# Performance work log

Hardware: AMD Instinct MI355X
Metric: run time of the kernel (lower is better)

Reference implementation:

```python
import jax, jax.numpy as jnp
import numpy as np
from jax import lax

H = 64  # hidden_size

def _lstm_layer(x, w_ih, w_hh, b_ih, b_hh):
    # x: (B, T, in). PyTorch gate order [i, f, g, o]; gates = x@W_ih^T + h@W_hh^T + b_ih + b_hh.
    B, T, _ = x.shape
    xw = jnp.einsum('bti,gi->btg', x, w_ih) + (b_ih + b_hh)  # (B, T, 4H), input projection hoisted out of scan

    def step(carry, xw_t):
        h, c = carry
        gates = xw_t + h @ w_hh.T                     # (B, 4H)
        i, f, g, o = jnp.split(gates, 4, axis=-1)
        i = jax.nn.sigmoid(i)
        f = jax.nn.sigmoid(f)
        g = jnp.tanh(g)
        o = jax.nn.sigmoid(o)
        c = f * c + i * g
        h = o * jnp.tanh(c)
        return (h, c), h

    h0 = jnp.zeros((B, H), dtype=x.dtype)
    c0 = jnp.zeros((B, H), dtype=x.dtype)
    (h_n, _), hs = lax.scan(step, (h0, c0), jnp.swapaxes(xw, 0, 1))  # hs: (T, B, H)
    return jnp.swapaxes(hs, 0, 1), h_n


def setup_inputs() -> dict:
    key = jax.random.key(0)
    ks = jax.random.split(key, 12)
    s = 1.0 / np.sqrt(H)  # PyTorch LSTM init scale
    return {
        'x':     jax.random.normal(ks[0], (2048, 512, 4), dtype=jnp.float32),
        'w_ih0': jax.random.uniform(ks[1], (4 * H, 4), jnp.float32, -s, s),
        'w_hh0': jax.random.uniform(ks[2], (4 * H, H), jnp.float32, -s, s),
        'b_ih0': jax.random.uniform(ks[3], (4 * H,), jnp.float32, -s, s),
        'b_hh0': jax.random.uniform(ks[4], (4 * H,), jnp.float32, -s, s),
        'w_ih1': jax.random.uniform(ks[5], (4 * H, H), jnp.float32, -s, s),
        'w_hh1': jax.random.uniform(ks[6], (4 * H, H), jnp.float32, -s, s),
        'b_ih1': jax.random.uniform(ks[7], (4 * H,), jnp.float32, -s, s),
        'b_hh1': jax.random.uniform(ks[8], (4 * H,), jnp.float32, -s, s),
        'fc_w':  jax.random.uniform(ks[9], (H, H), jnp.float32, -s, s),
        'fc_b':  jax.random.uniform(ks[10], (H,), jnp.float32, -s, s),
    }


def reference(x, w_ih0, w_hh0, b_ih0, b_hh0, w_ih1, w_hh1, b_ih1, b_hh1, fc_w, fc_b):
    # 2-layer LSTM (eval mode: inter-layer dropout inactive), take last layer's final hidden,
    # then Linear + tanh.
    h1_seq, _ = _lstm_layer(x, w_ih0, w_hh0, b_ih0, b_hh0)
    _, h_n = _lstm_layer(h1_seq, w_ih1, w_hh1, b_ih1, b_hh1)
    return jnp.tanh(h_n @ fc_w.T + fc_b)
```

## Files before the change

kernel.cpp:

```cpp
#include <hip/hip_runtime.h>


#define HID 64
#define TSTEPS 512
#define MB 8
#define BLK 512
#define HSTR 72
#define LOG2E  1.4426950408889634f
#define LOG2E2 2.8853900817779268f

typedef _Float16 f16;
typedef _Float16 half8 __attribute__((ext_vector_type(8)));
typedef _Float16 half4 __attribute__((ext_vector_type(4)));
typedef float f32x4 __attribute__((ext_vector_type(4)));

__device__ __forceinline__ float sig2(float y) {
    return __builtin_amdgcn_rcpf(1.0f + __builtin_amdgcn_exp2f(-y));
}
__device__ __forceinline__ float tanh2(float y) {
    return fmaf(2.0f, __builtin_amdgcn_rcpf(1.0f + __builtin_amdgcn_exp2f(-y)), -1.0f);
}

__global__ __launch_bounds__(BLK, 2) void lstm_mfma(
    const float* __restrict__ x,
    const float* __restrict__ w_ih0,
    const float* __restrict__ w_hh0,
    const float* __restrict__ b_ih0,
    const float* __restrict__ b_hh0,
    const float* __restrict__ w_ih1,
    const float* __restrict__ w_hh1,
    const float* __restrict__ b_ih1,
    const float* __restrict__ b_hh1,
    const float* __restrict__ fc_w,
    const float* __restrict__ fc_b,
    float* __restrict__ out)
{
    __shared__ f16 xs[TSTEPS * MB * 4];
    __shared__ f16 h0s[2][MB * HSTR];
    __shared__ f16 h1s[MB * HSTR];

    const int tid  = threadIdx.x;
    const int w    = tid >> 6;
    const int l    = tid & 63;
    const int quad = l >> 4;
    const int l15  = l & 15;
    const int wl   = w & 3;
    const bool isL0 = (w < 4);
    const int b0   = blockIdx.x * MB;

    for (int it = tid; it < MB * TSTEPS; it += BLK) {
        const int m = it >> 9;
        const int t = it & 511;
        const float4 v = *((const float4*)x + (size_t)(b0 + m) * TSTEPS + t);
        *(half4*)(xs + (t * MB + m) * 4) =
            (half4){ (f16)v.x, (f16)v.y, (f16)v.z, (f16)v.w };
    }
    for (int it = tid; it < MB * HSTR; it += BLK) {
        h0s[0][it] = (f16)0.f; h0s[1][it] = (f16)0.f; h1s[it] = (f16)0.f;
    }

    half8 Bf[4][4];
    float biasr[4];
    const half8 Z = { (f16)0.f,(f16)0.f,(f16)0.f,(f16)0.f,
                      (f16)0.f,(f16)0.f,(f16)0.f,(f16)0.f };
    #pragma unroll
    for (int ti = 0; ti < 4; ++ti) {
        const int n = (wl + 4 * ti) * 16 + l15;
        const float sc = (ti == 2) ? LOG2E2 : LOG2E;
        if (isL0) {
            biasr[ti] = (b_ih0[n] + b_hh0[n]) * sc;
            half8 pz = Z;
            if (quad == 0) {
                const float4 v = *(const float4*)(w_ih0 + n * 4);
                pz[0] = (f16)(v.x * sc); pz[1] = (f16)(v.y * sc);
                pz[2] = (f16)(v.z * sc); pz[3] = (f16)(v.w * sc);
            }
            Bf[ti][0] = pz;
            #pragma unroll
            for (int ks = 0; ks < 2; ++ks) {
                const int ko = ks * 32 + quad * 8;
                const float4 a = *(const float4*)(w_hh0 + n * HID + ko);
                const float4 b = *(const float4*)(w_hh0 + n * HID + ko + 4);
                Bf[ti][1 + ks] = (half8){
                    (f16)(a.x*sc),(f16)(a.y*sc),(f16)(a.z*sc),(f16)(a.w*sc),
                    (f16)(b.x*sc),(f16)(b.y*sc),(f16)(b.z*sc),(f16)(b.w*sc) };
            }
            Bf[ti][3] = Z;
        } else {
            biasr[ti] = (b_ih1[n] + b_hh1[n]) * sc;
            #pragma unroll
            for (int ks = 0; ks < 2; ++ks) {
                const int ko = ks * 32 + quad * 8;
                const float4 a = *(const float4*)(w_ih1 + n * HID + ko);
                const float4 b = *(const float4*)(w_ih1 + n * HID + ko + 4);
                Bf[ti][ks] = (half8){
                    (f16)(a.x*sc),(f16)(a.y*sc),(f16)(a.z*sc),(f16)(a.w*sc),
                    (f16)(b.x*sc),(f16)(b.y*sc),(f16)(b.z*sc),(f16)(b.w*sc) };
                const float4 c = *(const float4*)(w_hh1 + n * HID + ko);
                const float4 d = *(const float4*)(w_hh1 + n * HID + ko + 4);
                Bf[ti][2 + ks] = (half8){
                    (f16)(c.x*sc),(f16)(c.y*sc),(f16)(c.z*sc),(f16)(c.w*sc),
                    (f16)(d.x*sc),(f16)(d.y*sc),(f16)(d.z*sc),(f16)(d.w*sc) };
            }
        }
    }

    const bool lo   = (quad < 2);
    const int  mrow = (quad & 1) * 4 + (lo ? 0 : 2);
    const int  uu   = wl * 16 + l15;
    const int  hb   = (l15 & 7) * HSTR + quad * 8;
    float cst0 = 0.f, cst1 = 0.f;
    f32x4 g[4];

    auto l0_mfma = [&](int r, const f16* h0rd) {
        const half4 xv = *(const half4*)(xs + (r * MB + (l15 & 7)) * 4);
        half8 ax = Z;
        if (quad == 0) { ax[0]=xv[0]; ax[1]=xv[1]; ax[2]=xv[2]; ax[3]=xv[3]; }
        const half8 A1 = *(const half8*)(h0rd + hb);
        const half8 A2 = *(const half8*)(h0rd + hb + 32);
        #pragma unroll
        for (int ti = 0; ti < 4; ++ti) {
            f32x4 acc = { biasr[ti], biasr[ti], biasr[ti], biasr[ti] };
            acc   = __builtin_amdgcn_mfma_f32_16x16x32_f16(ax, Bf[ti][0], acc, 0, 0, 0);
            acc   = __builtin_amdgcn_mfma_f32_16x16x32_f16(A1, Bf[ti][1], acc, 0, 0, 0);
            g[ti] = __builtin_amdgcn_mfma_f32_16x16x32_f16(A2, Bf[ti][2], acc, 0, 0, 0);
        }
    };
    auto l1_mfma = [&](const f16* h0rd) {
        const half8 A1 = *(const half8*)(h0rd + hb);
        const half8 A2 = *(const half8*)(h0rd + hb + 32);
        const half8 A3 = *(const half8*)(h1s + hb);
        const half8 A4 = *(const half8*)(h1s + hb + 32);
        #pragma unroll
        for (int ti = 0; ti < 4; ++ti) {
            f32x4 acc = { biasr[ti], biasr[ti], biasr[ti], biasr[ti] };
            acc   = __builtin_amdgcn_mfma_f32_16x16x32_f16(A1, Bf[ti][0], acc, 0, 0, 0);
            acc   = __builtin_amdgcn_mfma_f32_16x16x32_f16(A2, Bf[ti][1], acc, 0, 0, 0);
            acc   = __builtin_amdgcn_mfma_f32_16x16x32_f16(A3, Bf[ti][2], acc, 0, 0, 0);
            g[ti] = __builtin_amdgcn_mfma_f32_16x16x32_f16(A4, Bf[ti][3], acc, 0, 0, 0);
        }
    };
    auto act_store = [&](f16* dst) {
        #pragma unroll
        for (int j = 0; j < 2; ++j) {
            const float pi = lo ? g[0][j] : g[0][2 + j];
            const float pf = lo ? g[1][j] : g[1][2 + j];
            const float pg = lo ? g[2][j] : g[2][2 + j];
            const float po = lo ? g[3][j] : g[3][2 + j];
            float& c = j ? cst1 : cst0;
            c = sig2(pf) * c + sig2(pi) * tanh2(pg);
            dst[(mrow + j) * HSTR + uu] = (f16)(sig2(po) * tanh2(c * LOG2E2));
        }
    };

    __syncthreads();

    if (isL0) l0_mfma(0, h0s[1]);
    __syncthreads();
    if (isL0) act_store(h0s[0]);
    __syncthreads();
    if (isL0) l0_mfma(1, h0s[0]);
    __syncthreads();
    if (isL0) act_store(h0s[1]);
    else      l1_mfma(h0s[0]);
    __syncthreads();

    #pragma unroll 1
    for (int r = 2; r < TSTEPS; r += 2) {
        if (isL0) l0_mfma(r, h0s[1]);
        else      act_store(h1s);
        __syncthreads();
        if (isL0) act_store(h0s[0]);
        else      l1_mfma(h0s[1]);
        __syncthreads();
        if (isL0) l0_mfma(r + 1, h0s[0]);
        else      act_store(h1s);
        __syncthreads();
        if (isL0) act_store(h0s[1]);
        else      l1_mfma(h0s[0]);
        __syncthreads();
    }

    if (!isL0) act_store(h1s);
    __syncthreads();
    if (!isL0) l1_mfma(h0s[1]);
    __syncthreads();
    if (!isL0) act_store(h1s);
    __syncthreads();

    {
        const int v = tid & 63;
        const int m = tid >> 6;
        float a = fc_b[v];
        const f16* hp = h1s + m * HSTR;
        const float4* wp = (const float4*)(fc_w + v * HID);
        #pragma unroll
        for (int kk = 0; kk < HID / 4; ++kk) {
            const float4 wv = wp[kk];
            a += (float)hp[kk * 4 + 0] * wv.x + (float)hp[kk * 4 + 1] * wv.y
               + (float)hp[kk * 4 + 2] * wv.z + (float)hp[kk * 4 + 3] * wv.w;
        }
        out[(size_t)(b0 + m) * HID + v] = tanh2(a * LOG2E2);
    }
}

extern "C" void kernel_launch(void* const* d_in, const int* in_sizes, int n_in,
                              void* d_out, int out_size, void* d_ws, size_t ws_size,
                              hipStream_t stream) {
    const float* x     = (const float*)d_in[0];
    const float* w_ih0 = (const float*)d_in[1];
    const float* w_hh0 = (const float*)d_in[2];
    const float* b_ih0 = (const float*)d_in[3];
    const float* b_hh0 = (const float*)d_in[4];
    const float* w_ih1 = (const float*)d_in[5];
    const float* w_hh1 = (const float*)d_in[6];
    const float* b_ih1 = (const float*)d_in[7];
    const float* b_hh1 = (const float*)d_in[8];
    const float* fc_w  = (const float*)d_in[9];
    const float* fc_b  = (const float*)d_in[10];
    float* out = (float*)d_out;

    const int B = in_sizes[0] / (TSTEPS * 4);
    lstm_mfma<<<dim3(B / MB), dim3(BLK), 0, stream>>>(
        x, w_ih0, w_hh0, b_ih0, b_hh0, w_ih1, w_hh1, b_ih1, b_hh1, fc_w, fc_b, out);
}
```

Baseline: 399.5 us.

## Double-buffer layer-1 hidden state to halve barriers per timestep

Double-buffers the layer-1 hidden state so each wavefront can run its MFMA and activation/store back-to-back, needing one block barrier per timestep instead of two. Remaps A-operand row indices (RM) so each lane's needed batch rows land in accumulator elements 0-1, removing the lo/hi select in the activation. Passes the bias vector directly as the MFMA accumulator input. This cuts synchronization overhead on the serial recurrence, at the cost of extra shared memory and duplicated rows within each MFMA tile.

```diff
diff --git a/kernel.cpp b/kernel.cpp
--- a/kernel.cpp
+++ b/kernel.cpp
@@ -37,7 +37,7 @@
 {
     __shared__ f16 xs[TSTEPS * MB * 4];
     __shared__ f16 h0s[2][MB * HSTR];
-    __shared__ f16 h1s[MB * HSTR];
+    __shared__ f16 h1s[2][MB * HSTR];
 
     const int tid  = threadIdx.x;
     const int w    = tid >> 6;
@@ -48,6 +48,8 @@
     const bool isL0 = (w < 4);
     const int b0   = blockIdx.x * MB;
 
+    const int RM = (l15 < 8) ? l15 : ((l15 & 4) | ((l15 + 2) & 3));
+
     for (int it = tid; it < MB * TSTEPS; it += BLK) {
         const int m = it >> 9;
         const int t = it & 511;
@@ -56,19 +58,21 @@
             (half4){ (f16)v.x, (f16)v.y, (f16)v.z, (f16)v.w };
     }
     for (int it = tid; it < MB * HSTR; it += BLK) {
-        h0s[0][it] = (f16)0.f; h0s[1][it] = (f16)0.f; h1s[it] = (f16)0.f;
+        h0s[0][it] = (f16)0.f; h0s[1][it] = (f16)0.f;
+        h1s[0][it] = (f16)0.f; h1s[1][it] = (f16)0.f;
     }
 
     half8 Bf[4][4];
-    float biasr[4];
+    f32x4 biasv[4];
     const half8 Z = { (f16)0.f,(f16)0.f,(f16)0.f,(f16)0.f,
                       (f16)0.f,(f16)0.f,(f16)0.f,(f16)0.f };
     #pragma unroll
     for (int ti = 0; ti < 4; ++ti) {
         const int n = (wl + 4 * ti) * 16 + l15;
         const float sc = (ti == 2) ? LOG2E2 : LOG2E;
+        float bval;
         if (isL0) {
-            biasr[ti] = (b_ih0[n] + b_hh0[n]) * sc;
+            bval = (b_ih0[n] + b_hh0[n]) * sc;
             half8 pz = Z;
             if (quad == 0) {
                 const float4 v = *(const float4*)(w_ih0 + n * 4);
@@ -87,7 +91,7 @@
             }
             Bf[ti][3] = Z;
         } else {
-            biasr[ti] = (b_ih1[n] + b_hh1[n]) * sc;
+            bval = (b_ih1[n] + b_hh1[n]) * sc;
             #pragma unroll
             for (int ks = 0; ks < 2; ++ks) {
                 const int ko = ks * 32 + quad * 8;
@@ -103,38 +107,38 @@
                     (f16)(d.x*sc),(f16)(d.y*sc),(f16)(d.z*sc),(f16)(d.w*sc) };
             }
         }
-    }
-
-    const bool lo   = (quad < 2);
-    const int  mrow = (quad & 1) * 4 + (lo ? 0 : 2);
+        biasv[ti] = (f32x4){ bval, bval, bval, bval };
+    }
+
+    const int  mrow = (quad & 1) * 4 + (quad & 2);
     const int  uu   = wl * 16 + l15;
-    const int  hb   = (l15 & 7) * HSTR + quad * 8;
+    const int  hb   = RM * HSTR + quad * 8;
     float cst0 = 0.f, cst1 = 0.f;
     f32x4 g[4];
 
     auto l0_mfma = [&](int r, const f16* h0rd) {
-        const half4 xv = *(const half4*)(xs + (r * MB + (l15 & 7)) * 4);
+        const half4 xv = *(const half4*)(xs + (r * MB + RM) * 4);
         half8 ax = Z;
         if (quad == 0) { ax[0]=xv[0]; ax[1]=xv[1]; ax[2]=xv[2]; ax[3]=xv[3]; }
         const half8 A1 = *(const half8*)(h0rd + hb);
         const half8 A2 = *(const half8*)(h0rd + hb + 32);
         #pragma unroll
         for (int ti = 0; ti < 4; ++ti) {
-            f32x4 acc = { biasr[ti], biasr[ti], biasr[ti], biasr[ti] };
-            acc   = __builtin_amdgcn_mfma_f32_16x16x32_f16(ax, Bf[ti][0], acc, 0, 0, 0);
+            f32x4 acc;
+            acc   = __builtin_amdgcn_mfma_f32_16x16x32_f16(ax, Bf[ti][0], biasv[ti], 0, 0, 0);
             acc   = __builtin_amdgcn_mfma_f32_16x16x32_f16(A1, Bf[ti][1], acc, 0, 0, 0);
             g[ti] = __builtin_amdgcn_mfma_f32_16x16x32_f16(A2, Bf[ti][2], acc, 0, 0, 0);
         }
     };
-    auto l1_mfma = [&](const f16* h0rd) {
+    auto l1_mfma = [&](const f16* h0rd, const f16* h1rd) {
         const half8 A1 = *(const half8*)(h0rd + hb);
         const half8 A2 = *(const half8*)(h0rd + hb + 32);
-        const half8 A3 = *(const half8*)(h1s + hb);
-        const half8 A4 = *(const half8*)(h1s + hb + 32);
+        const half8 A3 = *(const half8*)(h1rd + hb);
+        const half8 A4 = *(const half8*)(h1rd + hb + 32);
         #pragma unroll
         for (int ti = 0; ti < 4; ++ti) {
-            f32x4 acc = { biasr[ti], biasr[ti], biasr[ti], biasr[ti] };
-            acc   = __builtin_amdgcn_mfma_f32_16x16x32_f16(A1, Bf[ti][0], acc, 0, 0, 0);
+            f32x4 acc;
+            acc   = __builtin_amdgcn_mfma_f32_16x16x32_f16(A1, Bf[ti][0], biasv[ti], 0, 0, 0);
             acc   = __builtin_amdgcn_mfma_f32_16x16x32_f16(A2, Bf[ti][1], acc, 0, 0, 0);
             acc   = __builtin_amdgcn_mfma_f32_16x16x32_f16(A3, Bf[ti][2], acc, 0, 0, 0);
             g[ti] = __builtin_amdgcn_mfma_f32_16x16x32_f16(A4, Bf[ti][3], acc, 0, 0, 0);
@@ -143,10 +147,7 @@
     auto act_store = [&](f16* dst) {
         #pragma unroll
         for (int j = 0; j < 2; ++j) {
-            const float pi = lo ? g[0][j] : g[0][2 + j];
-            const float pf = lo ? g[1][j] : g[1][2 + j];
-            const float pg = lo ? g[2][j] : g[2][2 + j];
-            const float po = lo ? g[3][j] : g[3][2 + j];
+            const float pi = g[0][j], pf = g[1][j], pg = g[2][j], po = g[3][j];
             float& c = j ? cst1 : cst0;
             c = sig2(pf) * c + sig2(pi) * tanh2(pg);
             dst[(mrow + j) * HSTR + uu] = (f16)(sig2(po) * tanh2(c * LOG2E2));
@@ -155,44 +156,35 @@
 
     __syncthreads();
 
-    if (isL0) l0_mfma(0, h0s[1]);
-    __syncthreads();
-    if (isL0) act_store(h0s[0]);
-    __syncthreads();
-    if (isL0) l0_mfma(1, h0s[0]);
-    __syncthreads();
-    if (isL0) act_store(h0s[1]);
-    else      l1_mfma(h0s[0]);
+    if (isL0) { l0_mfma(0, h0s[1]); act_store(h0s[0]); }
+    __syncthreads();
+    if (isL0) { l0_mfma(1, h0s[0]); act_store(h0s[1]); }
+    else      { l1_mfma(h0s[0], h1s[1]); act_store(h1s[0]); }
     __syncthreads();
 
     #pragma unroll 1
-    for (int r = 2; r < TSTEPS; r += 2) {
-        if (isL0) l0_mfma(r, h0s[1]);
-        else      act_store(h1s);
+    for (int r = 2; r < 510; r += 2) {
+        if (isL0) { l0_mfma(r, h0s[1]); act_store(h0s[0]); }
+        else      { l1_mfma(h0s[1], h1s[0]); act_store(h1s[1]); }
         __syncthreads();
-        if (isL0) act_store(h0s[0]);
-        else      l1_mfma(h0s[1]);
+        if (isL0) { l0_mfma(r + 1, h0s[0]); act_store(h0s[1]); }
+        else      { l1_mfma(h0s[0], h1s[1]); act_store(h1s[0]); }
         __syncthreads();
-        if (isL0) l0_mfma(r + 1, h0s[0]);
-        else      act_store(h1s);
-        __syncthreads();
-        if (isL0) act_store(h0s[1]);
-        else      l1_mfma(h0s[0]);
-        __syncthreads();
-    }
-
-    if (!isL0) act_store(h1s);
-    __syncthreads();
-    if (!isL0) l1_mfma(h0s[1]);
-    __syncthreads();
-    if (!isL0) act_store(h1s);
+    }
+    if (isL0) { l0_mfma(510, h0s[1]); act_store(h0s[0]); }
+    else      { l1_mfma(h0s[1], h1s[0]); act_store(h1s[1]); }
+    __syncthreads();
+    if (isL0) { l0_mfma(511, h0s[0]); act_store(h0s[1]); }
+    else      { l1_mfma(h0s[0], h1s[1]); act_store(h1s[0]); }
+    __syncthreads();
+    if (!isL0) { l1_mfma(h0s[1], h1s[0]); act_store(h1s[1]); }
     __syncthreads();
 
     {
         const int v = tid & 63;
         const int m = tid >> 6;
         float a = fc_b[v];
-        const f16* hp = h1s + m * HSTR;
+        const f16* hp = h1s[1] + m * HSTR;
         const float4* wp = (const float4*)(fc_w + v * HID);
         #pragma unroll
         for (int kk = 0; kk < HID / 4; ++kk) {
```

Measured after the change: 332.5 us. 16.8% less time.
